# Optimization experiments

Measured on AMD Instinct MI355X. Metric: run time of the kernel, lower is better.

Reference implementation:

```python
import jax, jax.numpy as jnp
import numpy as np

DIM = 256
N_HEADS = 4
B, N = 2, 4096


def setup_inputs() -> dict:
    key = jax.random.key(0)
    ks = jax.random.split(key, 10)
    s = DIM ** -0.5
    return {
        "x": jax.random.normal(ks[0], (B, N, DIM), dtype=jnp.float32),
        "q_w": jax.random.normal(ks[1], (DIM, DIM), dtype=jnp.float32) * s,
        "q_b": jnp.zeros((DIM,), dtype=jnp.float32),
        "k_w": jax.random.normal(ks[2], (DIM, DIM), dtype=jnp.float32) * s,
        "k_b": jnp.zeros((DIM,), dtype=jnp.float32),
        "v_w": jax.random.normal(ks[3], (DIM, DIM), dtype=jnp.float32) * s,
        "v_b": jnp.zeros((DIM,), dtype=jnp.float32),
        "o_w": jax.random.normal(ks[4], (DIM, DIM), dtype=jnp.float32) * s,
        "o_b": jnp.zeros((DIM,), dtype=jnp.float32),
        "tau": jnp.ones((1,), dtype=jnp.float32),
    }


def reference(x, q_w, q_b, k_w, k_b, v_w, v_b, o_w, o_b, tau):
    Bsz, Nlen, C = x.shape
    H = N_HEADS
    Dh = C // H
    scale = C ** -0.5  # source uses full dim, not head_dim
    Q = (x @ q_w.T + q_b).reshape(Bsz, Nlen, H, Dh)
    K = (x @ k_w.T + k_b).reshape(Bsz, Nlen, H, Dh)
    V = (x @ v_w.T + v_b).reshape(Bsz, Nlen, H, Dh)
    attn = jnp.einsum('bnhd,bmhd->bhnm', Q, K) * scale
    # soft-threshold gate: keep only |attn| > tau, then relu
    attn = jax.nn.relu(jnp.where(jnp.abs(attn) > tau, attn, 0.0))
    attn = jax.nn.softmax(attn, axis=-1)
    out = jnp.einsum('bhnm,bmhd->bnhd', attn, V).reshape(Bsz, Nlen, C)
    return out @ o_w.T + o_b
```

## Files before the change

### kernel.cpp

```cpp
#include <hip/hip_runtime.h>

#define SEQ   4096
#define CDIM  256
#define NHEAD 4
#define DHEAD 64
#define PSTRIDE 72

typedef float    f32x4 __attribute__((ext_vector_type(4)));
typedef _Float16 f16x8 __attribute__((ext_vector_type(8)));
typedef _Float16 f16x4 __attribute__((ext_vector_type(4)));

__device__ __forceinline__ f16x8 cvt_frag(const float* __restrict__ p) {
    float4 f0 = *(const float4*)p;
    float4 f1 = *(const float4*)(p + 4);
    f16x8 r;
    r[0]=(_Float16)f0.x; r[1]=(_Float16)f0.y; r[2]=(_Float16)f0.z; r[3]=(_Float16)f0.w;
    r[4]=(_Float16)f1.x; r[5]=(_Float16)f1.y; r[6]=(_Float16)f1.z; r[7]=(_Float16)f1.w;
    return r;
}

__global__ __launch_bounds__(256) void sta_prep(
    const float* __restrict__ qw, const float* __restrict__ kw,
    const float* __restrict__ vw, const float* __restrict__ ow,
    _Float16* __restrict__ w16)
{
    const int mat = blockIdx.y;
    const float* src = (mat == 0) ? qw : (mat == 1) ? kw : (mat == 2) ? vw : ow;
    const int i = (blockIdx.x * 256 + threadIdx.x) * 8;
    *(f16x8*)(w16 + mat * 65536 + i) = cvt_frag(src + i);
}

__global__ __launch_bounds__(256) void sta_qkv(
    const float* __restrict__ x, const _Float16* __restrict__ w16,
    const float* __restrict__ qb, const float* __restrict__ kb, const float* __restrict__ vb,
    _Float16* __restrict__ Qo, _Float16* __restrict__ Ko, _Float16* __restrict__ Vo)
{
    const int wave = threadIdx.x >> 6;
    const int lane = threadIdx.x & 63;
    const int l15  = lane & 15;
    const int quad = lane >> 4;
    const int mat  = blockIdx.y;
    const int half = blockIdx.z;
    const int row0 = blockIdx.x * 64 + wave * 16;

    const _Float16* w    = w16 + mat * 65536;
    const float*    bias = (mat == 0) ? qb : (mat == 1) ? kb : vb;

    f16x8 xf[8];
    const float* xrow = x + (row0 + l15) * CDIM + quad * 8;
    #pragma unroll
    for (int ks = 0; ks < 8; ks++) xf[ks] = cvt_frag(xrow + ks * 32);

    #pragma unroll 1
    for (int ct = 0; ct < 8; ct++) {
        const int ctg = half * 8 + ct;
        const _Float16* wr = w + (ctg * 16 + l15) * CDIM + quad * 8;
        f32x4 acc = {0.f, 0.f, 0.f, 0.f};
        if (mat < 2) {
            #pragma unroll
            for (int ks = 0; ks < 8; ks++)
                acc = __builtin_amdgcn_mfma_f32_16x16x32_f16(*(const f16x8*)(wr + ks * 32), xf[ks], acc, 0, 0, 0);
            const float4 bv = *(const float4*)(bias + ctg * 16 + quad * 4);
            const int c0 = ctg * 16 + quad * 4;
            const int h = c0 >> 6, d0 = c0 & 63;
            const int grow = row0 + l15, b = grow >> 12, n = grow & (SEQ - 1);
            const float sc = (mat == 0) ? 0.0625f : 1.0f;
            f16x4 o;
            o[0] = (_Float16)((acc[0] + bv.x) * sc);
            o[1] = (_Float16)((acc[1] + bv.y) * sc);
            o[2] = (_Float16)((acc[2] + bv.z) * sc);
            o[3] = (_Float16)((acc[3] + bv.w) * sc);
            _Float16* dst = ((mat == 0) ? Qo : Ko) + (((b * NHEAD + h) * SEQ + n) * DHEAD + d0);
            *(f16x4*)dst = o;
        } else {
            #pragma unroll
            for (int ks = 0; ks < 8; ks++)
                acc = __builtin_amdgcn_mfma_f32_16x16x32_f16(xf[ks], *(const f16x8*)(wr + ks * 32), acc, 0, 0, 0);
            const int c = ctg * 16 + l15;
            const int h = c >> 6, d = c & 63;
            const float bv = bias[c];
            const int grow0 = row0 + quad * 4, b = grow0 >> 12, n0 = grow0 & (SEQ - 1);
            f16x4 o;
            #pragma unroll
            for (int r = 0; r < 4; r++) o[r] = (_Float16)(acc[r] + bv);
            *(f16x4*)(Vo + (((b * NHEAD + h) * DHEAD + d) * SEQ + n0)) = o;
        }
    }
}

__global__ __launch_bounds__(64) void sta_attn(
    const _Float16* __restrict__ Q, const _Float16* __restrict__ K, const _Float16* __restrict__ Vt,
    const float* __restrict__ taup,
    float* __restrict__ Opart, float* __restrict__ lpart)
{
    __shared__ __align__(16) _Float16 pbuf[64 * PSTRIDE];

    const int lane = threadIdx.x;
    const int l15  = lane & 15;
    const int quad = lane >> 4;
    const int qt = blockIdx.x;
    const int bh = blockIdx.y;
    const int sp = blockIdx.z;
    const float tau_eff = fmaxf(taup[0], 0.0f);

    const _Float16* Qb = Q  + bh * SEQ * DHEAD;
    const _Float16* Kb = K  + bh * SEQ * DHEAD;
    const _Float16* Vb = Vt + bh * DHEAD * SEQ;

    const int q0 = qt * 64;

    f16x8 qf[4][2];
    #pragma unroll
    for (int qb = 0; qb < 4; qb++)
        #pragma unroll
        for (int ks = 0; ks < 2; ks++)
            qf[qb][ks] = *(const f16x8*)(Qb + (q0 + qb * 16 + l15) * DHEAD + ks * 32 + quad * 8);

    f32x4 O[4][4];
    #pragma unroll
    for (int qb = 0; qb < 4; qb++)
        #pragma unroll
        for (int db = 0; db < 4; db++) O[qb][db] = (f32x4){0.f, 0.f, 0.f, 0.f};
    float rs[4] = {0.f, 0.f, 0.f, 0.f};

    #pragma unroll 1
    for (int kt = sp * 16; kt < sp * 16 + 16; kt++) {
        const int kv0 = kt * 64;

        #pragma unroll
        for (int kb = 0; kb < 4; kb++) {
            const _Float16* kp = Kb + (kv0 + kb * 16 + l15) * DHEAD + quad * 8;
            f16x8 k0 = *(const f16x8*)kp;
            f16x8 k1 = *(const f16x8*)(kp + 32);
            #pragma unroll
            for (int qb = 0; qb < 4; qb++) {
                f32x4 a = {0.f, 0.f, 0.f, 0.f};
                a = __builtin_amdgcn_mfma_f32_16x16x32_f16(k0, qf[qb][0], a, 0, 0, 0);
                a = __builtin_amdgcn_mfma_f32_16x16x32_f16(k1, qf[qb][1], a, 0, 0, 0);
                f16x4 pk;
                float acc = 0.f;
                #pragma unroll
                for (int r = 0; r < 4; r++) {
                    float e = __expf(a[r]);
                    float p = (a[r] > tau_eff) ? e : 1.0f;
                    acc += p;
                    pk[r] = (_Float16)p;
                }
                rs[qb] += acc;
                *(f16x4*)(pbuf + (qb * 16 + l15) * PSTRIDE + kb * 16 + quad * 4) = pk;
            }
        }

        #pragma unroll
        for (int ks = 0; ks < 2; ks++) {
            f16x8 pa[4];
            #pragma unroll
            for (int qb = 0; qb < 4; qb++)
                pa[qb] = *(const f16x8*)(pbuf + (qb * 16 + l15) * PSTRIDE + ks * 32 + quad * 8);
            #pragma unroll
            for (int db = 0; db < 4; db++) {
                f16x8 vf = *(const f16x8*)(Vb + (db * 16 + l15) * SEQ + kv0 + ks * 32 + quad * 8);
                #pragma unroll
                for (int qb = 0; qb < 4; qb++)
                    O[qb][db] = __builtin_amdgcn_mfma_f32_16x16x32_f16(pa[qb], vf, O[qb][db], 0, 0, 0);
            }
        }
    }

    #pragma unroll
    for (int qb = 0; qb < 4; qb++) {
        float v = rs[qb];
        v += __shfl_xor(v, 16);
        v += __shfl_xor(v, 32);
        rs[qb] = v;
    }
    float* Ob = Opart + (size_t)((sp * 8 + bh) * SEQ + q0) * DHEAD;
    #pragma unroll
    for (int qb = 0; qb < 4; qb++)
        #pragma unroll
        for (int db = 0; db < 4; db++)
            #pragma unroll
            for (int r = 0; r < 4; r++)
                Ob[(qb * 16 + quad * 4 + r) * DHEAD + db * 16 + l15] = O[qb][db][r];
    if (quad == 0) {
        #pragma unroll
        for (int qb = 0; qb < 4; qb++)
            lpart[(sp * 8 + bh) * SEQ + q0 + qb * 16 + l15] = rs[qb];
    }
}

__global__ __launch_bounds__(256) void sta_combine(
    const float* __restrict__ Opart, const float* __restrict__ lpart,
    _Float16* __restrict__ AO)
{
    const int idx = blockIdx.x * 256 + threadIdx.x;
    const int dg = idx & 15, n = (idx >> 4) & (SEQ - 1), bh = idx >> 16;
    const int d0 = dg * 4;
    float4 o = {0.f, 0.f, 0.f, 0.f};
    float l = 0.f;
    #pragma unroll
    for (int s = 0; s < 4; s++) {
        const float4 os = *(const float4*)(Opart + (size_t)((s * 8 + bh) * SEQ + n) * DHEAD + d0);
        o.x += os.x; o.y += os.y; o.z += os.z; o.w += os.w;
        l += lpart[(s * 8 + bh) * SEQ + n];
    }
    const float inv = 1.0f / l;
    const int b = bh >> 2, h = bh & 3;
    f16x4 res;
    res[0] = (_Float16)(o.x * inv); res[1] = (_Float16)(o.y * inv);
    res[2] = (_Float16)(o.z * inv); res[3] = (_Float16)(o.w * inv);
    *(f16x4*)(AO + (size_t)(b * SEQ + n) * CDIM + h * DHEAD + d0) = res;
}

__global__ __launch_bounds__(256) void sta_oproj(
    const _Float16* __restrict__ AO, const _Float16* __restrict__ w16o,
    const float* __restrict__ ob, float* __restrict__ out)
{
    const int wave = threadIdx.x >> 6;
    const int lane = threadIdx.x & 63;
    const int l15  = lane & 15;
    const int quad = lane >> 4;
    const int row0 = blockIdx.x * 64 + wave * 16;
    const int quarter = blockIdx.y;

    f16x8 af[8];
    const _Float16* arow = AO + (row0 + l15) * CDIM + quad * 8;
    #pragma unroll
    for (int ks = 0; ks < 8; ks++) af[ks] = *(const f16x8*)(arow + ks * 32);

    #pragma unroll 1
    for (int ct = 0; ct < 4; ct++) {
        const int ctg = quarter * 4 + ct;
        const _Float16* wr = w16o + (ctg * 16 + l15) * CDIM + quad * 8;
        f32x4 acc = {0.f, 0.f, 0.f, 0.f};
        #pragma unroll
        for (int ks = 0; ks < 8; ks++)
            acc = __builtin_amdgcn_mfma_f32_16x16x32_f16(*(const f16x8*)(wr + ks * 32), af[ks], acc, 0, 0, 0);
        const float4 bv = *(const float4*)(ob + ctg * 16 + quad * 4);
        const int c0 = ctg * 16 + quad * 4;
        float4 res;
        res.x = acc[0] + bv.x; res.y = acc[1] + bv.y;
        res.z = acc[2] + bv.z; res.w = acc[3] + bv.w;
        *(float4*)(out + (size_t)(row0 + l15) * CDIM + c0) = res;
    }
}

extern "C" void kernel_launch(void* const* d_in, const int* in_sizes, int n_in,
                              void* d_out, int out_size, void* d_ws, size_t ws_size,
                              hipStream_t stream) {
    const float* x   = (const float*)d_in[0];
    const float* qw  = (const float*)d_in[1];
    const float* qb  = (const float*)d_in[2];
    const float* kw  = (const float*)d_in[3];
    const float* kb  = (const float*)d_in[4];
    const float* vw  = (const float*)d_in[5];
    const float* vb  = (const float*)d_in[6];
    const float* ow  = (const float*)d_in[7];
    const float* ob  = (const float*)d_in[8];
    const float* tau = (const float*)d_in[9];

    _Float16* w16 = (_Float16*)d_ws;
    _Float16* Q   = w16 + 262144;
    _Float16* K   = Q + 2097152;
    _Float16* Vt  = K + 2097152;
    _Float16* AO  = Vt + 2097152;
    float* Opart  = (float*)(AO + 2097152);
    float* lpart  = Opart + 8388608;

    sta_prep   <<<dim3(32, 4),      256, 0, stream>>>(qw, kw, vw, ow, w16);
    sta_qkv    <<<dim3(128, 3, 2),  256, 0, stream>>>(x, w16, qb, kb, vb, Q, K, Vt);
    sta_attn   <<<dim3(64, 8, 4),    64, 0, stream>>>(Q, K, Vt, tau, Opart, lpart);
    sta_combine<<<2048,             256, 0, stream>>>(Opart, lpart, AO);
    sta_oproj  <<<dim3(128, 4),     256, 0, stream>>>(AO, ow ? (w16 + 3 * 65536) : (w16 + 3 * 65536), ob, (float*)d_out);
}
```

Baseline: 207.9 us.

## Fuse split-KV combine into output projection with fp16 partials and 8-way split

Raises the KV split from 4 to 8 blocks per query tile, stores the attention partial outputs in fp16 instead of fp32, and accumulates the row sums with atomics into a zeroed buffer. The separate combine kernel is removed: the output projection now sums the eight fp16 partials and scales by the reciprocal row sum while loading its A operand. This trades a kernel launch and an fp32 round-trip for more attention blocks and more partial reads in the projection. Summing partials and applying the normalisation in fp16 adds rounding and overflow risk.

```diff
diff --git a/kernel.cpp b/kernel.cpp
--- a/kernel.cpp
+++ b/kernel.cpp
@@ -5,6 +5,7 @@
 #define NHEAD 4
 #define DHEAD 64
 #define PSTRIDE 72
+#define NSPLIT 8
 
 typedef float    f32x4 __attribute__((ext_vector_type(4)));
 typedef _Float16 f16x8 __attribute__((ext_vector_type(8)));
@@ -91,7 +92,7 @@
 __global__ __launch_bounds__(64) void sta_attn(
     const _Float16* __restrict__ Q, const _Float16* __restrict__ K, const _Float16* __restrict__ Vt,
     const float* __restrict__ taup,
-    float* __restrict__ Opart, float* __restrict__ lpart)
+    _Float16* __restrict__ Opart, float* __restrict__ lfull)
 {
     __shared__ __align__(16) _Float16 pbuf[64 * PSTRIDE];
 
@@ -124,7 +125,7 @@
     float rs[4] = {0.f, 0.f, 0.f, 0.f};
 
     #pragma unroll 1
-    for (int kt = sp * 16; kt < sp * 16 + 16; kt++) {
+    for (int kt = sp * 8; kt < sp * 8 + 8; kt++) {
         const int kv0 = kt * 64;
 
         #pragma unroll
@@ -153,16 +154,16 @@
 
         #pragma unroll
         for (int ks = 0; ks < 2; ks++) {
-            f16x8 pa[4];
+            f16x8 pb[4];
             #pragma unroll
             for (int qb = 0; qb < 4; qb++)
-                pa[qb] = *(const f16x8*)(pbuf + (qb * 16 + l15) * PSTRIDE + ks * 32 + quad * 8);
+                pb[qb] = *(const f16x8*)(pbuf + (qb * 16 + l15) * PSTRIDE + ks * 32 + quad * 8);
             #pragma unroll
             for (int db = 0; db < 4; db++) {
                 f16x8 vf = *(const f16x8*)(Vb + (db * 16 + l15) * SEQ + kv0 + ks * 32 + quad * 8);
                 #pragma unroll
                 for (int qb = 0; qb < 4; qb++)
-                    O[qb][db] = __builtin_amdgcn_mfma_f32_16x16x32_f16(pa[qb], vf, O[qb][db], 0, 0, 0);
+                    O[qb][db] = __builtin_amdgcn_mfma_f32_16x16x32_f16(vf, pb[qb], O[qb][db], 0, 0, 0);
             }
         }
     }
@@ -174,59 +175,57 @@
         v += __shfl_xor(v, 32);
         rs[qb] = v;
     }
-    float* Ob = Opart + (size_t)((sp * 8 + bh) * SEQ + q0) * DHEAD;
-    #pragma unroll
-    for (int qb = 0; qb < 4; qb++)
-        #pragma unroll
-        for (int db = 0; db < 4; db++)
-            #pragma unroll
-            for (int r = 0; r < 4; r++)
-                Ob[(qb * 16 + quad * 4 + r) * DHEAD + db * 16 + l15] = O[qb][db][r];
+    _Float16* Ob = Opart + (size_t)((sp * 8 + bh) * SEQ + q0) * DHEAD;
+    #pragma unroll
+    for (int qb = 0; qb < 4; qb++) {
+        #pragma unroll
+        for (int db = 0; db < 4; db++) {
+            f16x4 ov;
+            #pragma unroll
+            for (int r = 0; r < 4; r++) ov[r] = (_Float16)O[qb][db][r];
+            *(f16x4*)(Ob + (qb * 16 + l15) * DHEAD + db * 16 + quad * 4) = ov;
+        }
+    }
     if (quad == 0) {
         #pragma unroll
         for (int qb = 0; qb < 4; qb++)
-            lpart[(sp * 8 + bh) * SEQ + q0 + qb * 16 + l15] = rs[qb];
-    }
-}
-
-__global__ __launch_bounds__(256) void sta_combine(
-    const float* __restrict__ Opart, const float* __restrict__ lpart,
-    _Float16* __restrict__ AO)
-{
-    const int idx = blockIdx.x * 256 + threadIdx.x;
-    const int dg = idx & 15, n = (idx >> 4) & (SEQ - 1), bh = idx >> 16;
-    const int d0 = dg * 4;
-    float4 o = {0.f, 0.f, 0.f, 0.f};
-    float l = 0.f;
-    #pragma unroll
-    for (int s = 0; s < 4; s++) {
-        const float4 os = *(const float4*)(Opart + (size_t)((s * 8 + bh) * SEQ + n) * DHEAD + d0);
-        o.x += os.x; o.y += os.y; o.z += os.z; o.w += os.w;
-        l += lpart[(s * 8 + bh) * SEQ + n];
-    }
-    const float inv = 1.0f / l;
-    const int b = bh >> 2, h = bh & 3;
-    f16x4 res;
-    res[0] = (_Float16)(o.x * inv); res[1] = (_Float16)(o.y * inv);
-    res[2] = (_Float16)(o.z * inv); res[3] = (_Float16)(o.w * inv);
-    *(f16x4*)(AO + (size_t)(b * SEQ + n) * CDIM + h * DHEAD + d0) = res;
-}
-
-__global__ __launch_bounds__(256) void sta_oproj(
-    const _Float16* __restrict__ AO, const _Float16* __restrict__ w16o,
-    const float* __restrict__ ob, float* __restrict__ out)
+            atomicAdd(&lfull[bh * SEQ + q0 + qb * 16 + l15], rs[qb]);
+    }
+}
+
+__global__ __launch_bounds__(128) void sta_oproj(
+    const _Float16* __restrict__ Opart, const float* __restrict__ lfull,
+    const _Float16* __restrict__ w16o, const float* __restrict__ ob,
+    float* __restrict__ out)
 {
     const int wave = threadIdx.x >> 6;
     const int lane = threadIdx.x & 63;
     const int l15  = lane & 15;
     const int quad = lane >> 4;
-    const int row0 = blockIdx.x * 64 + wave * 16;
+    const int row0 = blockIdx.x * 32 + wave * 16;
     const int quarter = blockIdx.y;
 
+    const int grow = row0 + l15;
+    const int b = grow >> 12, n = grow & (SEQ - 1);
+
+    _Float16 inv[NHEAD];
+    #pragma unroll
+    for (int h = 0; h < NHEAD; h++)
+        inv[h] = (_Float16)(1.0f / lfull[(b * NHEAD + h) * SEQ + n]);
+
     f16x8 af[8];
-    const _Float16* arow = AO + (row0 + l15) * CDIM + quad * 8;
-    #pragma unroll
-    for (int ks = 0; ks < 8; ks++) af[ks] = *(const f16x8*)(arow + ks * 32);
+    #pragma unroll
+    for (int ks = 0; ks < 8; ks++) {
+        const int hq = ks * 4 + quad;
+        const int h  = hq >> 3;
+        const int d0 = (hq & 7) * 8;
+        const _Float16* pp = Opart + (size_t)((b * NHEAD + h) * SEQ + n) * DHEAD + d0;
+        f16x8 s = *(const f16x8*)pp;
+        #pragma unroll
+        for (int sp = 1; sp < NSPLIT; sp++)
+            s = s + *(const f16x8*)(pp + (size_t)sp * 8 * SEQ * DHEAD);
+        af[ks] = s * inv[h];
+    }
 
     #pragma unroll 1
     for (int ct = 0; ct < 4; ct++) {
@@ -241,7 +240,7 @@
         float4 res;
         res.x = acc[0] + bv.x; res.y = acc[1] + bv.y;
         res.z = acc[2] + bv.z; res.w = acc[3] + bv.w;
-        *(float4*)(out + (size_t)(row0 + l15) * CDIM + c0) = res;
+        *(float4*)(out + (size_t)grow * CDIM + c0) = res;
     }
 }
 
@@ -263,13 +262,12 @@
     _Float16* Q   = w16 + 262144;
     _Float16* K   = Q + 2097152;
     _Float16* Vt  = K + 2097152;
-    _Float16* AO  = Vt + 2097152;
-    float* Opart  = (float*)(AO + 2097152);
-    float* lpart  = Opart + 8388608;
-
-    sta_prep   <<<dim3(32, 4),      256, 0, stream>>>(qw, kw, vw, ow, w16);
-    sta_qkv    <<<dim3(128, 3, 2),  256, 0, stream>>>(x, w16, qb, kb, vb, Q, K, Vt);
-    sta_attn   <<<dim3(64, 8, 4),    64, 0, stream>>>(Q, K, Vt, tau, Opart, lpart);
-    sta_combine<<<2048,             256, 0, stream>>>(Opart, lpart, AO);
-    sta_oproj  <<<dim3(128, 4),     256, 0, stream>>>(AO, ow ? (w16 + 3 * 65536) : (w16 + 3 * 65536), ob, (float*)d_out);
-}
+    _Float16* Opart = Vt + 2097152;
+    float* lfull  = (float*)(Opart + 16777216);
+
+    sta_prep <<<dim3(32, 4),     256, 0, stream>>>(qw, kw, vw, ow, w16);
+    sta_qkv  <<<dim3(128, 3, 2), 256, 0, stream>>>(x, w16, qb, kb, vb, Q, K, Vt);
+    hipMemsetAsync(lfull, 0, NHEAD * 2 * SEQ * sizeof(float), stream);
+    sta_attn <<<dim3(64, 8, 8),   64, 0, stream>>>(Q, K, Vt, tau, Opart, lfull);
+    sta_oproj<<<dim3(256, 4),    128, 0, stream>>>(Opart, lfull, w16 + 3 * 65536, ob, (float*)d_out);
+}
```

Measured after the change: 221.7 us. +6.7%, slower.
